# Kernel tuning notes

Hardware: AMD Instinct MI355X
Metric: run time of the kernel (lower is better)

## Reference

```python
import jax, jax.numpy as jnp
import numpy as np

NE, EW, TOP_K, T_D, MAXNNZ = 32, 2944, 4, 8, 256
ALPHA, LIMIT, ORIG = 1.702, 7.0, 2880
HID = 2048


def setup_inputs() -> dict:
    key = jax.random.key(0)
    ks = jax.random.split(key, 7)
    dt = jnp.float16
    hid = jax.random.normal(ks[0], (1, 1024, HID), dtype=dt)
    # rand_init() sets all params to torch.rand(...)/5 -> Uniform[0, 0.2)
    gate_w = (jax.random.uniform(ks[1], (NE, HID), dtype=dt) * 0.2).astype(dt)
    u = (jax.random.uniform(ks[2], (NE * EW, HID), dtype=dt) * 0.2).astype(dt)
    g = (jax.random.uniform(ks[3], (NE * EW, HID), dtype=dt) * 0.2).astype(dt)
    d = (jax.random.uniform(ks[4], (HID, NE * EW), dtype=dt) * 0.2).astype(dt)
    ub = (jax.random.uniform(ks[5], (NE * EW,), dtype=dt) * 0.2).astype(dt)
    gb = (jax.random.uniform(ks[6], (NE * EW,), dtype=dt) * 0.2).astype(dt)
    return {"hid": hid, "gate_w": gate_w, "u": u, "g": g, "d": d, "ub": ub, "gb": gb}


def _act(up, gate):
    # clamped GLU: gate clamped above, up clamped both sides; glu = g*sigmoid(alpha*g); (up+1)*glu
    gate = jnp.minimum(gate, LIMIT)
    up = jnp.clip(up, -LIMIT, LIMIT)
    glu = gate * jax.nn.sigmoid(gate * ALPHA)
    act = (up + 1.0) * glu
    return act.at[..., ORIG:].set(0)  # padded inter dims (2880..2944) zeroed


def _forward(hid, gate_w, u, g, d, ub, gb):
    B, S, H = hid.shape
    x = hid.reshape(-1, H)           # [bs, H]
    bs = x.shape[0]

    # --- routing: softmax -> top-k -> renormalize -> scatter to sparse weights ---
    logits = (x @ gate_w.T).astype(jnp.float32)          # [bs, NE]
    probs = jax.nn.softmax(logits, axis=1)
    vals, idx = jax.lax.top_k(probs, TOP_K)
    vals = vals / vals.sum(axis=1, keepdims=True)
    sparse_rw = jnp.zeros_like(probs).at[jnp.arange(bs)[:, None], idx].set(vals)
    rw = sparse_rw.astype(x.dtype)                        # [bs, NE]

    # --- expert selection: t_d dense experts + t_d sparse experts by load ---
    routing_n = jnp.count_nonzero(rw, axis=0)
    mask_c = jax.lax.top_k(routing_n, 2 * T_D)[1]         # [2*T_D]
    cd, cs = mask_c[:T_D], mask_c[T_D:]
    # top-MAXNNZ tokens per sparse expert
    mask_r = jax.lax.top_k(sparse_rw[:, cs].T, MAXNNZ)[1].T  # [MAXNNZ, T_D]

    U = u.reshape(NE, EW, H)
    G = g.reshape(NE, EW, H)
    UB = ub.reshape(NE, EW)
    GB = gb.reshape(NE, EW)
    D = d.reshape(H, NE, EW)

    # --- dense experts: every token runs through the t_d hottest experts ---
    up_d = jnp.einsum('nh,teh->nte', x, U[cd]) + UB[cd]   # [bs, T_D, EW]
    gt_d = jnp.einsum('nh,teh->nte', x, G[cd]) + GB[cd]
    act_d = _act(up_d, gt_d) * rw[:, cd][..., None]       # routing weight combine
    out = jnp.einsum('nte,hte->nh', act_d, D[:, cd])      # [bs, H]

    # --- sparse experts: gather top-MAXNNZ tokens, MLP, scatter-add back ---
    xs = x[mask_r]                                        # [M, T_D, H]
    up_s = jnp.einsum('mth,teh->mte', xs, U[cs]) + UB[cs]
    gt_s = jnp.einsum('mth,teh->mte', xs, G[cs]) + GB[cs]
    w_s = rw[mask_r, cs[None, :]]                         # [M, T_D]
    act_s = _act(up_s, gt_s) * w_s[..., None]
    contrib = jnp.einsum('mte,hte->mth', act_s, D[:, cs])  # [M, T_D, H]
    out = out.at[mask_r.reshape(-1)].add(contrib.reshape(-1, H))

    return out.reshape(B, S, H)


def reference(hid, gate_w, u, g, d, ub, gb):
    return _forward(hid, gate_w, u, g, d, ub, gb)
```

## Files before the change

kernel.cpp:

```cpp
#include <hip/hip_runtime.h>

#define HID 2048
#define NE_ 32
#define EW_ 2944
#define ORIG_ 2880
#define TOPK_ 4
#define MAXNNZ_ 256
#define BS_ 1024
#define NEWTOT (NE_*EW_)
#define LDSP 40

typedef unsigned short u16;
typedef _Float16 h8  __attribute__((ext_vector_type(8)));
typedef float  f32x4 __attribute__((ext_vector_type(4)));
typedef float  fv4   __attribute__((ext_vector_type(4)));
typedef short  s16x8 __attribute__((ext_vector_type(8)));

__device__ __forceinline__ u16 f2h_bits(float f){
  union{ _Float16 h; u16 u; } c; c.h = (_Float16)f; return c.u;
}
__device__ __forceinline__ float f16q(float f){ return (float)(_Float16)f; }

__device__ __forceinline__ h8 cvt8(fv4 a, fv4 b){
  h8 r;
  r[0]=(_Float16)a[0]; r[1]=(_Float16)a[1]; r[2]=(_Float16)a[2]; r[3]=(_Float16)a[3];
  r[4]=(_Float16)b[0]; r[5]=(_Float16)b[1]; r[6]=(_Float16)b[2]; r[7]=(_Float16)b[3];
  return r;
}
__device__ __forceinline__ int ldsx(int row, int q8){ return row*LDSP + q8*8; }

__global__ __launch_bounds__(256) void k_gate(const float* __restrict__ x,
                                              const float* __restrict__ gw,
                                              float* __restrict__ rw,
                                              float* __restrict__ rwf,
                                              int* __restrict__ counts)
{
  __shared__ float slog[4][NE_];
  const int tid = threadIdx.x, wid = tid>>6, lane = tid&63;
  const int n = blockIdx.x*4 + wid;
  const float* xr = x + (size_t)n*HID + lane*32;
  float xf[32];
  #pragma unroll
  for (int i=0;i<8;i++){
    fv4 v = *(const fv4*)(xr + i*4);
    #pragma unroll
    for (int j=0;j<4;j++) xf[i*4+j] = v[j];
  }
  for (int e=0;e<NE_;e++){
    const float* gr = gw + (size_t)e*HID + lane*32;
    float p = 0.f;
    #pragma unroll
    for (int i=0;i<8;i++){
      fv4 v = *(const fv4*)(gr + i*4);
      #pragma unroll
      for (int j=0;j<4;j++) p += xf[i*4+j]*v[j];
    }
    #pragma unroll
    for (int s=32;s>0;s>>=1) p += __shfl_xor(p, s);
    if (lane==0) slog[wid][e] = f16q(p);
  }
  if (lane==0){
    float mx=-1e30f;
    for (int e=0;e<NE_;e++) mx = fmaxf(mx, slog[wid][e]);
    float pr[NE_]; float sum=0.f;
    for (int e=0;e<NE_;e++){ float v=__expf(slog[wid][e]-mx); pr[e]=v; sum+=v; }
    for (int e=0;e<NE_;e++) pr[e] = pr[e]/sum;
    int   idx[TOPK_]; float val[TOPK_]; bool used[NE_];
    for (int e=0;e<NE_;e++) used[e]=false;
    float vs=0.f;
    for (int k=0;k<TOPK_;k++){
      float best=-1.f; int bi=0;
      for (int e=0;e<NE_;e++) if(!used[e] && pr[e]>best){best=pr[e];bi=e;}
      used[bi]=true; idx[k]=bi; val[k]=best; vs+=best;
    }
    float* rwr  = rw  + (size_t)n*NE_;
    float* rwfr = rwf + (size_t)n*NE_;
    for (int k=0;k<TOPK_;k++){
      float vraw = val[k]/vs;
      float q = f16q(vraw);
      rwr[idx[k]]  = q;
      rwfr[idx[k]] = vraw;
      if (q!=0.f) atomicAdd(counts+idx[k], 1);
    }
  }
}

__global__ void k_rank(const int* __restrict__ counts, int* __restrict__ cdcs)
{
  if (threadIdx.x==0){
    int cnt[NE_]; bool used[NE_];
    for (int e=0;e<NE_;e++){ cnt[e]=counts[e]; used[e]=false; }
    for (int k=0;k<16;k++){
      int best=-1, bi=0;
      for (int e=0;e<NE_;e++) if(!used[e] && cnt[e]>best){best=cnt[e];bi=e;}
      used[bi]=true; cdcs[k]=bi;
    }
  }
}

__global__ __launch_bounds__(256) void k_lists(const float* __restrict__ rw,
                                               const float* __restrict__ rwf,
                                               const int* __restrict__ cdcs,
                                               int* __restrict__ tok_all,
                                               int* __restrict__ cnt_all,
                                               int* __restrict__ inv,
                                               int* __restrict__ invcnt)
{
  __shared__ float v[BS_];
  __shared__ int scnt;
  const int z = blockIdx.x;
  const int e = cdcs[z];
  const int tid = threadIdx.x;
  for (int i=tid;i<BS_;i+=256) tok_all[z*BS_+i] = 0;
  for (int i=tid;i<BS_;i+=256) v[i] = (z<8) ? rw[(size_t)i*NE_+e] : rwf[(size_t)i*NE_+e];
  if (tid==0) scnt = 0;
  __syncthreads();
  for (int i=tid;i<BS_;i+=256){
    bool take;
    if (z<8){
      take = (v[i]!=0.f);
    } else {
      float vi=v[i]; int r=0;
      for (int m=0;m<BS_;m++){
        float vm=v[m];
        r += (vm>vi) || (vm==vi && m<i);
      }
      take = (r<MAXNNZ_) && (rw[(size_t)i*NE_+e]!=0.f);
    }
    if (take){
      int slot = atomicAdd(&scnt,1);
      tok_all[z*BS_+slot] = i;
      int c = atomicAdd(&invcnt[i],1);
      inv[i*4+c] = (z<<16) | slot;
    }
  }
  __syncthreads();
  if (tid==0) cnt_all[z] = scnt;
}

__global__ __launch_bounds__(256) void k_fused(const float* __restrict__ x,
                                               const float* __restrict__ uw,
                                               const float* __restrict__ gww,
                                               const float* __restrict__ ub,
                                               const float* __restrict__ gb,
                                               const float* __restrict__ rw,
                                               const int* __restrict__ cdcs,
                                               const int* __restrict__ tok_all,
                                               const int* __restrict__ cnt_all,
                                               u16* __restrict__ act)
{
  const int z=blockIdx.z, bx=blockIdx.x, by=blockIdx.y;
  const int cnt = cnt_all[z];
  if (by*128 >= cnt) return;
  const int e = cdcs[z];
  __shared__ __align__(16) u16 ldsA[2][128*LDSP];
  __shared__ __align__(16) u16 ldsB[2][128*LDSP];
  const int tid=threadIdx.x, lane=tid&63, w=tid>>6;
  const int wr=w>>1, wc=w&1;

  const int ar = tid>>2, ach = tid&3;
  const int tokA0 = tok_all[z*BS_ + by*128 + ar];
  const int tokA1 = tok_all[z*BS_ + by*128 + ar + 64];
  const float* ap0 = x + (size_t)tokA0*HID + ach*8;
  const float* ap1 = x + (size_t)tokA1*HID + ach*8;
  const float* bp0 = uw  + ((size_t)e*EW_ + bx*64 + ar)*HID + ach*8;
  const float* bp1 = gww + ((size_t)e*EW_ + bx*64 + ar)*HID + ach*8;

  f32x4 au[4][2], ag[4][2];
  #pragma unroll
  for (int i=0;i<4;i++)
    #pragma unroll
    for (int j=0;j<2;j++)
      #pragma unroll
      for (int q=0;q<4;q++){ au[i][j][q]=0.f; ag[i][j][q]=0.f; }

  fv4 aR00=*(const fv4*)ap0, aR01=*(const fv4*)(ap0+4);
  fv4 aR10=*(const fv4*)ap1, aR11=*(const fv4*)(ap1+4);
  fv4 bR00=*(const fv4*)bp0, bR01=*(const fv4*)(bp0+4);
  fv4 bR10=*(const fv4*)bp1, bR11=*(const fv4*)(bp1+4);
  const int NK = HID/32;
  for (int kt=0; kt<NK; kt++){
    u16* A = ldsA[kt&1]; u16* B = ldsB[kt&1];
    *(h8*)&A[ldsx(ar,    ach)] = cvt8(aR00,aR01);
    *(h8*)&A[ldsx(ar+64, ach)] = cvt8(aR10,aR11);
    *(h8*)&B[ldsx(ar,    ach)] = cvt8(bR00,bR01);
    *(h8*)&B[ldsx(ar+64, ach)] = cvt8(bR10,bR11);
    if (kt+1<NK){
      const int k1=(kt+1)*32;
      aR00=*(const fv4*)(ap0+k1); aR01=*(const fv4*)(ap0+k1+4);
      aR10=*(const fv4*)(ap1+k1); aR11=*(const fv4*)(ap1+k1+4);
      bR00=*(const fv4*)(bp0+k1); bR01=*(const fv4*)(bp0+k1+4);
      bR10=*(const fv4*)(bp1+k1); bR11=*(const fv4*)(bp1+k1+4);
    }
    __syncthreads();
    const int kq = lane>>4;
    const u16* Ar = ldsA[kt&1]; const u16* Br = ldsB[kt&1];
    h8 af[4], fu[2], fg[2];
    #pragma unroll
    for (int m=0;m<4;m++) af[m] = *(const h8*)&Ar[ldsx(wr*64+m*16+(lane&15), kq)];
    #pragma unroll
    for (int n2=0;n2<2;n2++){
      fu[n2] = *(const h8*)&Br[ldsx(wc*32+n2*16+(lane&15), kq)];
      fg[n2] = *(const h8*)&Br[ldsx(64+wc*32+n2*16+(lane&15), kq)];
    }
    #pragma unroll
    for (int m=0;m<4;m++)
      #pragma unroll
      for (int n2=0;n2<2;n2++){
        au[m][n2]=__builtin_amdgcn_mfma_f32_16x16x32_f16(af[m],fu[n2],au[m][n2],0,0,0);
        ag[m][n2]=__builtin_amdgcn_mfma_f32_16x16x32_f16(af[m],fg[n2],ag[m][n2],0,0,0);
      }
  }

  #pragma unroll
  for (int n2=0;n2<2;n2++){
    const int col = bx*64 + wc*32 + n2*16 + (lane&15);
    const float ubv = ub[(size_t)e*EW_ + col];
    const float gbv = gb[(size_t)e*EW_ + col];
    #pragma unroll
    for (int m=0;m<4;m++){
      #pragma unroll
      for (int j=0;j<4;j++){
        const int s = by*128 + wr*64 + m*16 + (lane>>4)*4 + j;
        float upv = f16q(au[m][n2][j] + ubv);
        float gtv = f16q(ag[m][n2][j] + gbv);
        float wv = 0.f;
        if (s < cnt) wv = rw[(size_t)tok_all[z*BS_+s]*NE_ + e];
        float gc = fminf(gtv, 7.0f);
        float uc = fminf(fmaxf(upv,-7.0f),7.0f);
        float glu = gc * (1.f/(1.f+__expf(-gc*1.702f)));
        act[((size_t)z*BS_+s)*ORIG_ + col] = f2h_bits((uc+1.f)*glu*wv);
      }
    }
  }
}

__global__ __launch_bounds__(256) void k_down(const u16* __restrict__ act,
                                              const float* __restrict__ dw,
                                              const int* __restrict__ cdcs,
                                              const int* __restrict__ cnt_all,
                                              float* __restrict__ contrib)
{
  const int zz=blockIdx.z, bx=blockIdx.x, by=blockIdx.y;
  const int z = zz>>1, kh = zz&1;
  const int cnt = cnt_all[z];
  if (by*128 >= cnt) return;
  const int e = cdcs[z];
  __shared__ __align__(16) u16 ldsA[2][128*LDSP];
  __shared__ __align__(16) u16 ldsB[2][128*LDSP];
  const int tid=threadIdx.x, lane=tid&63, w=tid>>6;
  const int wr=w>>1, wc=w&1;
  const int ar = tid>>2, ach = tid&3;
  const int kbase = kh*1440;

  const u16* ap0 = act + ((size_t)z*BS_ + by*128 + ar)*ORIG_ + kbase + ach*8;
  const u16* ap1 = ap0 + (size_t)64*ORIG_;
  const float* bp0 = dw + (size_t)(bx*128 + ar)*NEWTOT + (size_t)e*EW_ + kbase + ach*8;
  const float* bp1 = bp0 + (size_t)64*NEWTOT;

  f32x4 acc[4][4];
  #pragma unroll
  for (int i=0;i<4;i++)
    #pragma unroll
    for (int j=0;j<4;j++)
      #pragma unroll
      for (int q=0;q<4;q++) acc[i][j][q]=0.f;

  s16x8 ra0 = *(const s16x8*)ap0;
  s16x8 ra1 = *(const s16x8*)ap1;
  fv4 bR00=*(const fv4*)bp0, bR01=*(const fv4*)(bp0+4);
  fv4 bR10=*(const fv4*)bp1, bR11=*(const fv4*)(bp1+4);
  const int NK = 1440/32;
  for (int kt=0; kt<NK; kt++){
    u16* A = ldsA[kt&1]; u16* B = ldsB[kt&1];
    *(s16x8*)&A[ldsx(ar,    ach)] = ra0;
    *(s16x8*)&A[ldsx(ar+64, ach)] = ra1;
    *(h8*)&B[ldsx(ar,    ach)] = cvt8(bR00,bR01);
    *(h8*)&B[ldsx(ar+64, ach)] = cvt8(bR10,bR11);
    if (kt+1<NK){
      const int k1 = (kt+1)*32;
      ra0 = *(const s16x8*)(ap0 + k1);
      ra1 = *(const s16x8*)(ap1 + k1);
      bR00=*(const fv4*)(bp0+k1); bR01=*(const fv4*)(bp0+k1+4);
      bR10=*(const fv4*)(bp1+k1); bR11=*(const fv4*)(bp1+k1+4);
    }
    __syncthreads();
    const int kq = lane>>4;
    const u16* Ar = ldsA[kt&1]; const u16* Br = ldsB[kt&1];
    h8 af[4], bfr[4];
    #pragma unroll
    for (int m=0;m<4;m++)    af[m]  = *(const h8*)&Ar[ldsx(wr*64+m*16+(lane&15), kq)];
    #pragma unroll
    for (int n2=0;n2<4;n2++) bfr[n2] = *(const h8*)&Br[ldsx(wc*64+n2*16+(lane&15), kq)];
    #pragma unroll
    for (int m=0;m<4;m++)
      #pragma unroll
      for (int n2=0;n2<4;n2++)
        acc[m][n2]=__builtin_amdgcn_mfma_f32_16x16x32_f16(af[m],bfr[n2],acc[m][n2],0,0,0);
  }

  #pragma unroll
  for (int m=0;m<4;m++){
    #pragma unroll
    for (int j=0;j<4;j++){
      const int slot = by*128 + wr*64 + m*16 + (lane>>4)*4 + j;
      #pragma unroll
      for (int n2=0;n2<4;n2++){
        const int col = bx*128 + wc*64 + n2*16 + (lane&15);
        contrib[((size_t)zz*BS_ + slot)*HID + col] = acc[m][n2][j];
      }
    }
  }
}

__global__ __launch_bounds__(256) void k_combine(const float* __restrict__ contrib,
                                                 const int* __restrict__ inv,
                                                 const int* __restrict__ invcnt,
                                                 float* __restrict__ out)
{
  const int gid = blockIdx.x*256 + threadIdx.x;
  const int base = gid*4;
  const int n = base >> 11;
  const int h = base & 2047;
  fv4 acc = {0.f,0.f,0.f,0.f};
  const int c = invcnt[n];
  for (int j=0;j<c;j++){
    const int code = inv[n*4+j];
    const int z = code>>16;
    const int slot = code & 0xFFFF;
    const float* p = contrib + ((size_t)(z*2)*BS_ + slot)*HID + h;
    acc += *(const fv4*)p;
    acc += *(const fv4*)(p + (size_t)BS_*HID);
  }
  *(fv4*)(out + base) = acc;
}

extern "C" void kernel_launch(void* const* d_in, const int* in_sizes, int n_in,
                              void* d_out, int out_size, void* d_ws, size_t ws_size,
                              hipStream_t stream)
{
  const float* x  = (const float*)d_in[0];
  const float* gw = (const float*)d_in[1];
  const float* u  = (const float*)d_in[2];
  const float* g  = (const float*)d_in[3];
  const float* dw = (const float*)d_in[4];
  const float* ub = (const float*)d_in[5];
  const float* gb = (const float*)d_in[6];

  char* ws = (char*)d_ws;
  size_t off = 0;
  auto alloc = [&](size_t bytes)->void*{ void* p = ws + off; off += (bytes + 255) & ~(size_t)255; return p; };
  float* rw     = (float*)alloc((size_t)BS_*NE_*4);
  float* rwf    = (float*)alloc((size_t)BS_*NE_*4);
  int*   counts = (int*)  alloc(NE_*4);
  int*   invcnt = (int*)  alloc(BS_*4);
  size_t zero_span = off;
  int*   cdcs   = (int*)  alloc(16*4);
  int*   cnt_all= (int*)  alloc(16*4);
  int*   tok_all= (int*)  alloc((size_t)16*BS_*4);
  int*   inv    = (int*)  alloc((size_t)BS_*4*4);
  u16*   act    = (u16*)  alloc((size_t)16*BS_*ORIG_*2);
  float* contrib= (float*)alloc((size_t)32*BS_*HID*4);
  if (off > ws_size) return;

  hipMemsetAsync(ws, 0, zero_span, stream);

  k_gate <<<BS_/4, 256, 0, stream>>>(x, gw, rw, rwf, counts);
  k_rank <<<1,     64,  0, stream>>>(counts, cdcs);
  k_lists<<<16,    256, 0, stream>>>(rw, rwf, cdcs, tok_all, cnt_all, inv, invcnt);

  k_fused<<<dim3(ORIG_/64, 8, 16), 256, 0, stream>>>(x, u, g, ub, gb, rw,
                                                     cdcs, tok_all, cnt_all, act);
  k_down <<<dim3(HID/128, 8, 32), 256, 0, stream>>>(act, dw, cdcs, cnt_all, contrib);
  k_combine<<<(BS_*HID/4)/256, 256, 0, stream>>>(contrib, inv, invcnt, (float*)d_out);
}
```

Baseline: 642.4 us.

## Retile expert GEMMs to 256-token tiles, pre-convert x to fp16, store contrib in fp16

Both expert GEMMs now use tiles that are 256 tokens tall and narrow in the weight dimension (32 columns each for up and gate, 64 for down). Each fp32 weight row is therefore read and converted by fewer blocks, which cuts the dominant weight traffic. A separate kernel converts x to fp16 once, so the fused kernel no longer converts activations on every load. The down-projection partial results are written in fp16 and rows past the valid count are skipped, which halves contrib traffic at some cost in precision for the partial sums.

```diff
diff --git a/kernel.cpp b/kernel.cpp
--- a/kernel.cpp
+++ b/kernel.cpp
@@ -14,10 +14,12 @@
 typedef _Float16 h8  __attribute__((ext_vector_type(8)));
 typedef float  f32x4 __attribute__((ext_vector_type(4)));
 typedef float  fv4   __attribute__((ext_vector_type(4)));
-typedef short  s16x8 __attribute__((ext_vector_type(8)));
 
 __device__ __forceinline__ u16 f2h_bits(float f){
   union{ _Float16 h; u16 u; } c; c.h = (_Float16)f; return c.u;
+}
+__device__ __forceinline__ float h2f_bits(u16 u){
+  union{ _Float16 h; u16 u; } c; c.u = u; return (float)c.h;
 }
 __device__ __forceinline__ float f16q(float f){ return (float)(_Float16)f; }
 
@@ -28,6 +30,14 @@
   return r;
 }
 __device__ __forceinline__ int ldsx(int row, int q8){ return row*LDSP + q8*8; }
+
+__global__ __launch_bounds__(256) void k_xcvt(const float* __restrict__ x,
+                                              u16* __restrict__ xh)
+{
+  const int base = (blockIdx.x*256 + threadIdx.x)*8;
+  fv4 a = *(const fv4*)(x+base), b = *(const fv4*)(x+base+4);
+  *(h8*)(xh+base) = cvt8(a,b);
+}
 
 __global__ __launch_bounds__(256) void k_gate(const float* __restrict__ x,
                                               const float* __restrict__ gw,
@@ -138,7 +148,7 @@
   if (tid==0) cnt_all[z] = scnt;
 }
 
-__global__ __launch_bounds__(256) void k_fused(const float* __restrict__ x,
+__global__ __launch_bounds__(256) void k_fused(const u16* __restrict__ xh,
                                                const float* __restrict__ uw,
                                                const float* __restrict__ gww,
                                                const float* __restrict__ ub,
@@ -151,20 +161,22 @@
 {
   const int z=blockIdx.z, bx=blockIdx.x, by=blockIdx.y;
   const int cnt = cnt_all[z];
-  if (by*128 >= cnt) return;
+  if (by*256 >= cnt) return;
   const int e = cdcs[z];
-  __shared__ __align__(16) u16 ldsA[2][128*LDSP];
-  __shared__ __align__(16) u16 ldsB[2][128*LDSP];
+  __shared__ __align__(16) u16 ldsA[2][256*LDSP];
+  __shared__ __align__(16) u16 ldsB[2][64*LDSP];
   const int tid=threadIdx.x, lane=tid&63, w=tid>>6;
-  const int wr=w>>1, wc=w&1;
 
   const int ar = tid>>2, ach = tid&3;
-  const int tokA0 = tok_all[z*BS_ + by*128 + ar];
-  const int tokA1 = tok_all[z*BS_ + by*128 + ar + 64];
-  const float* ap0 = x + (size_t)tokA0*HID + ach*8;
-  const float* ap1 = x + (size_t)tokA1*HID + ach*8;
-  const float* bp0 = uw  + ((size_t)e*EW_ + bx*64 + ar)*HID + ach*8;
-  const float* bp1 = gww + ((size_t)e*EW_ + bx*64 + ar)*HID + ach*8;
+  const u16* ap[4];
+  #pragma unroll
+  for (int r=0;r<4;r++){
+    const int tok = tok_all[z*BS_ + by*256 + ar + r*64];
+    ap[r] = xh + (size_t)tok*HID + ach*8;
+  }
+  const int br = tid>>2;
+  const float* bp = (br<32 ? uw  + ((size_t)e*EW_ + bx*32 + br)*HID
+                           : gww + ((size_t)e*EW_ + bx*32 + (br-32))*HID) + ach*8;
 
   f32x4 au[4][2], ag[4][2];
   #pragma unroll
@@ -174,34 +186,32 @@
       #pragma unroll
       for (int q=0;q<4;q++){ au[i][j][q]=0.f; ag[i][j][q]=0.f; }
 
-  fv4 aR00=*(const fv4*)ap0, aR01=*(const fv4*)(ap0+4);
-  fv4 aR10=*(const fv4*)ap1, aR11=*(const fv4*)(ap1+4);
-  fv4 bR00=*(const fv4*)bp0, bR01=*(const fv4*)(bp0+4);
-  fv4 bR10=*(const fv4*)bp1, bR11=*(const fv4*)(bp1+4);
+  h8 rA[4];
+  #pragma unroll
+  for (int r=0;r<4;r++) rA[r] = *(const h8*)ap[r];
+  fv4 rB0=*(const fv4*)bp, rB1=*(const fv4*)(bp+4);
   const int NK = HID/32;
   for (int kt=0; kt<NK; kt++){
     u16* A = ldsA[kt&1]; u16* B = ldsB[kt&1];
-    *(h8*)&A[ldsx(ar,    ach)] = cvt8(aR00,aR01);
-    *(h8*)&A[ldsx(ar+64, ach)] = cvt8(aR10,aR11);
-    *(h8*)&B[ldsx(ar,    ach)] = cvt8(bR00,bR01);
-    *(h8*)&B[ldsx(ar+64, ach)] = cvt8(bR10,bR11);
+    #pragma unroll
+    for (int r=0;r<4;r++) *(h8*)&A[ldsx(ar + r*64, ach)] = rA[r];
+    *(h8*)&B[ldsx(br, ach)] = cvt8(rB0,rB1);
     if (kt+1<NK){
       const int k1=(kt+1)*32;
-      aR00=*(const fv4*)(ap0+k1); aR01=*(const fv4*)(ap0+k1+4);
-      aR10=*(const fv4*)(ap1+k1); aR11=*(const fv4*)(ap1+k1+4);
-      bR00=*(const fv4*)(bp0+k1); bR01=*(const fv4*)(bp0+k1+4);
-      bR10=*(const fv4*)(bp1+k1); bR11=*(const fv4*)(bp1+k1+4);
+      #pragma unroll
+      for (int r=0;r<4;r++) rA[r] = *(const h8*)(ap[r]+k1);
+      rB0=*(const fv4*)(bp+k1); rB1=*(const fv4*)(bp+k1+4);
     }
     __syncthreads();
     const int kq = lane>>4;
     const u16* Ar = ldsA[kt&1]; const u16* Br = ldsB[kt&1];
     h8 af[4], fu[2], fg[2];
     #pragma unroll
-    for (int m=0;m<4;m++) af[m] = *(const h8*)&Ar[ldsx(wr*64+m*16+(lane&15), kq)];
+    for (int m=0;m<4;m++) af[m] = *(const h8*)&Ar[ldsx(w*64+m*16+(lane&15), kq)];
     #pragma unroll
     for (int n2=0;n2<2;n2++){
-      fu[n2] = *(const h8*)&Br[ldsx(wc*32+n2*16+(lane&15), kq)];
-      fg[n2] = *(const h8*)&Br[ldsx(64+wc*32+n2*16+(lane&15), kq)];
+      fu[n2] = *(const h8*)&Br[ldsx(n2*16+(lane&15), kq)];
+      fg[n2] = *(const h8*)&Br[ldsx(32+n2*16+(lane&15), kq)];
     }
     #pragma unroll
     for (int m=0;m<4;m++)
@@ -214,22 +224,23 @@
 
   #pragma unroll
   for (int n2=0;n2<2;n2++){
-    const int col = bx*64 + wc*32 + n2*16 + (lane&15);
+    const int col = bx*32 + n2*16 + (lane&15);
     const float ubv = ub[(size_t)e*EW_ + col];
     const float gbv = gb[(size_t)e*EW_ + col];
     #pragma unroll
     for (int m=0;m<4;m++){
       #pragma unroll
       for (int j=0;j<4;j++){
-        const int s = by*128 + wr*64 + m*16 + (lane>>4)*4 + j;
-        float upv = f16q(au[m][n2][j] + ubv);
-        float gtv = f16q(ag[m][n2][j] + gbv);
-        float wv = 0.f;
-        if (s < cnt) wv = rw[(size_t)tok_all[z*BS_+s]*NE_ + e];
-        float gc = fminf(gtv, 7.0f);
-        float uc = fminf(fmaxf(upv,-7.0f),7.0f);
-        float glu = gc * (1.f/(1.f+__expf(-gc*1.702f)));
-        act[((size_t)z*BS_+s)*ORIG_ + col] = f2h_bits((uc+1.f)*glu*wv);
+        const int s = by*256 + w*64 + m*16 + (lane>>4)*4 + j;
+        if (s < cnt){
+          float upv = f16q(au[m][n2][j] + ubv);
+          float gtv = f16q(ag[m][n2][j] + gbv);
+          float wv = rw[(size_t)tok_all[z*BS_+s]*NE_ + e];
+          float gc = fminf(gtv, 7.0f);
+          float uc = fminf(fmaxf(upv,-7.0f),7.0f);
+          float glu = gc * (1.f/(1.f+__expf(-gc*1.702f)));
+          act[((size_t)z*BS_+s)*ORIG_ + col] = f2h_bits((uc+1.f)*glu*wv);
+        }
       }
     }
   }
@@ -239,24 +250,24 @@
                                               const float* __restrict__ dw,
                                               const int* __restrict__ cdcs,
                                               const int* __restrict__ cnt_all,
-                                              float* __restrict__ contrib)
+                                              u16* __restrict__ contrib)
 {
   const int zz=blockIdx.z, bx=blockIdx.x, by=blockIdx.y;
   const int z = zz>>1, kh = zz&1;
   const int cnt = cnt_all[z];
-  if (by*128 >= cnt) return;
+  if (by*256 >= cnt) return;
   const int e = cdcs[z];
-  __shared__ __align__(16) u16 ldsA[2][128*LDSP];
-  __shared__ __align__(16) u16 ldsB[2][128*LDSP];
+  __shared__ __align__(16) u16 ldsA[2][256*LDSP];
+  __shared__ __align__(16) u16 ldsB[2][64*LDSP];
   const int tid=threadIdx.x, lane=tid&63, w=tid>>6;
-  const int wr=w>>1, wc=w&1;
   const int ar = tid>>2, ach = tid&3;
   const int kbase = kh*1440;
 
-  const u16* ap0 = act + ((size_t)z*BS_ + by*128 + ar)*ORIG_ + kbase + ach*8;
-  const u16* ap1 = ap0 + (size_t)64*ORIG_;
-  const float* bp0 = dw + (size_t)(bx*128 + ar)*NEWTOT + (size_t)e*EW_ + kbase + ach*8;
-  const float* bp1 = bp0 + (size_t)64*NEWTOT;
+  const u16* ap[4];
+  #pragma unroll
+  for (int r=0;r<4;r++)
+    ap[r] = act + ((size_t)z*BS_ + by*256 + ar + r*64)*ORIG_ + kbase + ach*8;
+  const float* bp = dw + (size_t)(bx*64 + ar)*NEWTOT + (size_t)e*EW_ + kbase + ach*8;
 
   f32x4 acc[4][4];
   #pragma unroll
@@ -266,32 +277,30 @@
       #pragma unroll
       for (int q=0;q<4;q++) acc[i][j][q]=0.f;
 
-  s16x8 ra0 = *(const s16x8*)ap0;
-  s16x8 ra1 = *(const s16x8*)ap1;
-  fv4 bR00=*(const fv4*)bp0, bR01=*(const fv4*)(bp0+4);
-  fv4 bR10=*(const fv4*)bp1, bR11=*(const fv4*)(bp1+4);
+  h8 rA[4];
+  #pragma unroll
+  for (int r=0;r<4;r++) rA[r] = *(const h8*)ap[r];
+  fv4 rB0=*(const fv4*)bp, rB1=*(const fv4*)(bp+4);
   const int NK = 1440/32;
   for (int kt=0; kt<NK; kt++){
     u16* A = ldsA[kt&1]; u16* B = ldsB[kt&1];
-    *(s16x8*)&A[ldsx(ar,    ach)] = ra0;
-    *(s16x8*)&A[ldsx(ar+64, ach)] = ra1;
-    *(h8*)&B[ldsx(ar,    ach)] = cvt8(bR00,bR01);
-    *(h8*)&B[ldsx(ar+64, ach)] = cvt8(bR10,bR11);
+    #pragma unroll
+    for (int r=0;r<4;r++) *(h8*)&A[ldsx(ar + r*64, ach)] = rA[r];
+    *(h8*)&B[ldsx(ar, ach)] = cvt8(rB0,rB1);
     if (kt+1<NK){
       const int k1 = (kt+1)*32;
-      ra0 = *(const s16x8*)(ap0 + k1);
-      ra1 = *(const s16x8*)(ap1 + k1);
-      bR00=*(const fv4*)(bp0+k1); bR01=*(const fv4*)(bp0+k1+4);
-      bR10=*(const fv4*)(bp1+k1); bR11=*(const fv4*)(bp1+k1+4);
+      #pragma unroll
+      for (int r=0;r<4;r++) rA[r] = *(const h8*)(ap[r]+k1);
+      rB0=*(const fv4*)(bp+k1); rB1=*(const fv4*)(bp+k1+4);
     }
     __syncthreads();
     const int kq = lane>>4;
     const u16* Ar = ldsA[kt&1]; const u16* Br = ldsB[kt&1];
     h8 af[4], bfr[4];
     #pragma unroll
-    for (int m=0;m<4;m++)    af[m]  = *(const h8*)&Ar[ldsx(wr*64+m*16+(lane&15), kq)];
-    #pragma unroll
-    for (int n2=0;n2<4;n2++) bfr[n2] = *(const h8*)&Br[ldsx(wc*64+n2*16+(lane&15), kq)];
+    for (int m=0;m<4;m++)    af[m]  = *(const h8*)&Ar[ldsx(w*64+m*16+(lane&15), kq)];
+    #pragma unroll
+    for (int n2=0;n2<4;n2++) bfr[n2] = *(const h8*)&Br[ldsx(n2*16+(lane&15), kq)];
     #pragma unroll
     for (int m=0;m<4;m++)
       #pragma unroll
@@ -303,36 +312,46 @@
   for (int m=0;m<4;m++){
     #pragma unroll
     for (int j=0;j<4;j++){
-      const int slot = by*128 + wr*64 + m*16 + (lane>>4)*4 + j;
-      #pragma unroll
-      for (int n2=0;n2<4;n2++){
-        const int col = bx*128 + wc*64 + n2*16 + (lane&15);
-        contrib[((size_t)zz*BS_ + slot)*HID + col] = acc[m][n2][j];
+      const int slot = by*256 + w*64 + m*16 + (lane>>4)*4 + j;
+      if (slot < cnt){
+        #pragma unroll
+        for (int n2=0;n2<4;n2++){
+          const int col = bx*64 + n2*16 + (lane&15);
+          contrib[((size_t)zz*BS_ + slot)*HID + col] = f2h_bits(acc[m][n2][j]);
+        }
       }
     }
   }
 }
 
-__global__ __launch_bounds__(256) void k_combine(const float* __restrict__ contrib,
+__global__ __launch_bounds__(256) void k_combine(const u16* __restrict__ contrib,
                                                  const int* __restrict__ inv,
                                                  const int* __restrict__ invcnt,
                                                  float* __restrict__ out)
 {
   const int gid = blockIdx.x*256 + threadIdx.x;
-  const int base = gid*4;
+  const int base = gid*8;
   const int n = base >> 11;
   const int h = base & 2047;
-  fv4 acc = {0.f,0.f,0.f,0.f};
+  float acc[8];
+  #pragma unroll
+  for (int q=0;q<8;q++) acc[q]=0.f;
   const int c = invcnt[n];
   for (int j=0;j<c;j++){
     const int code = inv[n*4+j];
     const int z = code>>16;
     const int slot = code & 0xFFFF;
-    const float* p = contrib + ((size_t)(z*2)*BS_ + slot)*HID + h;
-    acc += *(const fv4*)p;
-    acc += *(const fv4*)(p + (size_t)BS_*HID);
-  }
-  *(fv4*)(out + base) = acc;
+    const u16* p = contrib + ((size_t)(z*2)*BS_ + slot)*HID + h;
+    h8 v0 = *(const h8*)p;
+    h8 v1 = *(const h8*)(p + (size_t)BS_*HID);
+    #pragma unroll
+    for (int q=0;q<8;q++) acc[q] += (float)v0[q] + (float)v1[q];
+  }
+  fv4 o0, o1;
+  #pragma unroll
+  for (int q=0;q<4;q++){ o0[q]=acc[q]; o1[q]=acc[4+q]; }
+  *(fv4*)(out + base) = o0;
+  *(fv4*)(out + base + 4) = o1;
 }
 
 extern "C" void kernel_launch(void* const* d_in, const int* in_sizes, int n_in,
@@ -359,18 +378,20 @@
   int*   cnt_all= (int*)  alloc(16*4);
   int*   tok_all= (int*)  alloc((size_t)16*BS_*4);
   int*   inv    = (int*)  alloc((size_t)BS_*4*4);
+  u16*   xh     = (u16*)  alloc((size_t)BS_*HID*2);
   u16*   act    = (u16*)  alloc((size_t)16*BS_*ORIG_*2);
-  float* contrib= (float*)alloc((size_t)32*BS_*HID*4);
+  u16*   contrib= (u16*)  alloc((size_t)32*BS_*HID*2);
   if (off > ws_size) return;
 
   hipMemsetAsync(ws, 0, zero_span, stream);
 
+  k_xcvt <<<BS_*HID/(256*8), 256, 0, stream>>>(x, xh);
   k_gate <<<BS_/4, 256, 0, stream>>>(x, gw, rw, rwf, counts);
   k_rank <<<1,     64,  0, stream>>>(counts, cdcs);
   k_lists<<<16,    256, 0, stream>>>(rw, rwf, cdcs, tok_all, cnt_all, inv, invcnt);
 
-  k_fused<<<dim3(ORIG_/64, 8, 16), 256, 0, stream>>>(x, u, g, ub, gb, rw,
+  k_fused<<<dim3(ORIG_/32, 4, 16), 256, 0, stream>>>(xh, u, g, ub, gb, rw,
                                                      cdcs, tok_all, cnt_all, act);
-  k_down <<<dim3(HID/128, 8, 32), 256, 0, stream>>>(act, dw, cdcs, cnt_all, contrib);
-  k_combine<<<(BS_*HID/4)/256, 256, 0, stream>>>(contrib, inv, invcnt, (float*)d_out);
-}
+  k_down <<<dim3(HID/64, 4, 32), 256, 0, stream>>>(act, dw, cdcs, cnt_all, contrib);
+  k_combine<<<BS_*HID/(256*8), 256, 0, stream>>>(contrib, inv, invcnt, (float*)d_out);
+}
```

New measurement: 575.0 us. 1.12x faster.
